# Kernel optimization log

Hardware: AMD Instinct MI355X
Metric: run time of the kernel (lower is better)

Reference implementation:

```python
import jax, jax.numpy as jnp
import numpy as np

K_HOPS = 10
ALPHA = 0.1


def setup_inputs() -> dict:
    key = jax.random.key(0)
    ks = jax.random.split(key, 12)
    B, H, N, IC, F, C = 4096, 5, 30, 256, 512, 4
    real = jax.random.normal(ks[0], (B, N, IC), jnp.float32)
    imag = jax.random.normal(ks[1], (B, N, IC), jnp.float32)
    graph = jax.random.normal(ks[2], (B, H, N, N), jnp.float32)
    def lin(k, fan_in, shape):
        s = 1.0 / np.sqrt(fan_in)
        return jax.random.uniform(k, shape, jnp.float32, -s, s)
    W1 = lin(ks[3], IC, (IC, F)); b1 = lin(ks[4], IC, (F,))
    W2 = lin(ks[5], F, (F, F));  b2 = lin(ks[6], F, (F,))
    Wl = lin(ks[7], F, (F, 1));  bl = lin(ks[8], F, (1,))
    Wc = lin(ks[9], N, (C, N));  bc = lin(ks[10], N, (C,))
    return {"real": real, "imag": imag, "graph": graph,
            "W1": W1, "b1": b1, "W2": W2, "b2": b2,
            "Wl": Wl, "bl": bl, "Wc": Wc, "bc": bc}


def _appnp(S, x):
    # x_{k+1} = alpha * x0 + (1 - alpha) * S @ x_k, K iterations
    x0 = x
    def step(h, _):
        h = ALPHA * x0 + (1.0 - ALPHA) * jnp.einsum('bij,bjf->bif', S, h)
        return h, None
    h, _ = jax.lax.scan(step, x, None, length=K_HOPS)
    return h


def _prop_matrix(graph):
    # adj = mean over frequency dim; edges = nonzero entries (weights discarded
    # by the original code), self loops added, symmetric gcn_norm with
    # degree = column sums; source->target flow => operator is transposed.
    adj = jnp.mean(graph, axis=1)                      # [B,N,N]
    M = (adj != 0).astype(graph.dtype)
    N = M.shape[-1]
    Mt = M + jnp.eye(N, dtype=graph.dtype)             # add self loops
    deg = jnp.sum(Mt, axis=-2)                         # in-degree (col sums) [B,N]
    dinv = jax.lax.rsqrt(deg)
    S = dinv[:, :, None] * jnp.swapaxes(Mt, -1, -2) * dinv[:, None, :]
    return S


def reference(real, imag, graph, W1, b1, W2, b2, Wl, bl, Wc, bc):
    S = _prop_matrix(graph)
    # layer 1: linear -> relu -> APPNP(K=10)
    x = jax.nn.relu(jnp.einsum('bni,if->bnf', real, W1) + b1)
    x = _appnp(S, x)
    # layer 2: linear -> relu -> APPNP(K=10)
    x = jax.nn.relu(jnp.einsum('bnf,fg->bng', x, W2) + b2)
    x = _appnp(S, x)
    # readout: per-node linear to scalar, relu, then Conv1d(30->C, k=1)
    x = jax.nn.relu(jnp.einsum('bnf,fo->bno', x, Wl)[..., 0] + bl[0])  # [B,N]
    out = jnp.einsum('bn,cn->bc', x, Wc) + bc                          # [B,C]
    return out
```

## Files before the change

### kernel.cpp

```cpp
#include <hip/hip_runtime.h>
#include <hip/hip_bf16.h>

typedef _Float16 f16;
typedef _Float16 f16x8 __attribute__((ext_vector_type(8)));
typedef _Float16 f16x4 __attribute__((ext_vector_type(4)));
typedef float f32x4 __attribute__((ext_vector_type(4)));

#define P_OFF   0
#define W1T_OFF 14745600
#define W2T_OFF 15007744

__global__ __launch_bounds__(256) void k_prep(const float* __restrict__ W1,
                                              const float* __restrict__ W2,
                                              f16* __restrict__ w1t,
                                              f16* __restrict__ w2t) {
    long id = (long)blockIdx.x * 256 + threadIdx.x;
    if (id < 131072) {
        int f = (int)(id >> 8), k = (int)(id & 255);
        w1t[id] = (f16)W1[k * 512 + f];
    } else {
        long i = id - 131072;
        int f = (int)(i >> 9), k = (int)(i & 511);
        w2t[i] = (f16)W2[k * 512 + f];
    }
}

__global__ __launch_bounds__(256) void k_prop(const float* __restrict__ graph,
                                              float* __restrict__ P) {
    __shared__ float MtS[4][990];
    __shared__ float dinvS[4][32];
    __shared__ f16 qhS[4][1024];
    __shared__ f16 qlS[4][1024];

    const int wv = threadIdx.x >> 6, lane = threadIdx.x & 63;
    const int lr = lane & 15, gq = lane >> 4;
    const long b = (long)blockIdx.x * 4 + wv;
    const float* g = graph + b * 4500;
    float* Mt = MtS[wv];
    float* dinv = dinvS[wv];
    f16* qh = qhS[wv];
    f16* ql = qlS[wv];

    for (int rep = 0; rep < 15; ++rep) {
        int e = rep * 64 + lane;
        if (e < 900) {
            float s = g[e] + g[900 + e] + g[1800 + e] + g[2700 + e] + g[3600 + e];
            int r = e / 30, c = e - r * 30;
            Mt[r * 33 + c] = ((s != 0.f) ? 1.f : 0.f) + ((r == c) ? 1.f : 0.f);
        }
    }
    __syncthreads();
    if (lane < 30) {
        float d = 0.f;
        #pragma unroll
        for (int r = 0; r < 30; ++r) d += Mt[r * 33 + lane];
        dinv[lane] = 1.0f / sqrtf(d);
    }
    __syncthreads();

    auto Sval = [&](int i, int j) -> float {
        if (i >= 30 || j >= 30) return 0.f;
        return dinv[i] * Mt[j * 33 + i] * dinv[j];
    };

    f16x8 sh[2], sl[2];
    #pragma unroll
    for (int mi = 0; mi < 2; ++mi)
        #pragma unroll
        for (int jj = 0; jj < 8; ++jj) {
            float v = Sval(mi * 16 + lr, gq * 8 + jj);
            f16 h = (f16)v;
            sh[mi][jj] = h;
            sl[mi][jj] = (f16)(v - (float)h);
        }

    f32x4 qd[2][2], racc[2][2];
    #pragma unroll
    for (int mi = 0; mi < 2; ++mi)
        #pragma unroll
        for (int ni = 0; ni < 2; ++ni)
            #pragma unroll
            for (int r = 0; r < 4; ++r) {
                int row = mi * 16 + gq * 4 + r, col = ni * 16 + lr;
                qd[mi][ni][r] = Sval(row, col);
                racc[mi][ni][r] = (row == col) ? 0.1f : 0.f;
            }

    float c = 0.1f;
    for (int k = 1; k <= 9; ++k) {
        c *= 0.9f;
        #pragma unroll
        for (int mi = 0; mi < 2; ++mi)
            #pragma unroll
            for (int ni = 0; ni < 2; ++ni) {
                racc[mi][ni] += c * qd[mi][ni];
                f16x4 hh, ll;
                #pragma unroll
                for (int r = 0; r < 4; ++r) {
                    float v = qd[mi][ni][r];
                    f16 h = (f16)v;
                    hh[r] = h;
                    ll[r] = (f16)(v - (float)h);
                }
                const int col = ni * 16 + lr, rowb = mi * 16 + gq * 4;
                *reinterpret_cast<f16x4*>(qh + col * 32 + rowb) = hh;
                *reinterpret_cast<f16x4*>(ql + col * 32 + rowb) = ll;
            }
        __syncthreads();
        f16x8 bh[2], bl[2];
        #pragma unroll
        for (int ni = 0; ni < 2; ++ni) {
            const int col = ni * 16 + lr;
            bh[ni] = *reinterpret_cast<const f16x8*>(qh + col * 32 + gq * 8);
            bl[ni] = *reinterpret_cast<const f16x8*>(ql + col * 32 + gq * 8);
        }
        #pragma unroll
        for (int mi = 0; mi < 2; ++mi)
            #pragma unroll
            for (int ni = 0; ni < 2; ++ni) {
                f32x4 d = {0.f, 0.f, 0.f, 0.f};
                d = __builtin_amdgcn_mfma_f32_16x16x32_f16(sh[mi], bh[ni], d, 0, 0, 0);
                d = __builtin_amdgcn_mfma_f32_16x16x32_f16(sh[mi], bl[ni], d, 0, 0, 0);
                d = __builtin_amdgcn_mfma_f32_16x16x32_f16(sl[mi], bh[ni], d, 0, 0, 0);
                qd[mi][ni] = d;
            }
        __syncthreads();
    }
    const float cf = 0.3486784401f;
    #pragma unroll
    for (int mi = 0; mi < 2; ++mi)
        #pragma unroll
        for (int ni = 0; ni < 2; ++ni)
            #pragma unroll
            for (int r = 0; r < 4; ++r) {
                int row = mi * 16 + gq * 4 + r, col = ni * 16 + lr;
                if (row < 30 && col < 30)
                    P[b * 900 + row * 30 + col] = racc[mi][ni][r] + cf * qd[mi][ni][r];
            }
}

#define SMEM_BYTES 150496
#define PF_OFF   131072
#define B1L_OFF  139264
#define B2L_OFF  141312
#define WLL_OFF  143360
#define RED_OFF  145408
#define VL_OFF   149504
#define ZL_OFF   150016

__global__ __launch_bounds__(512, 2) void k_main(
    const float* __restrict__ real, const f16* __restrict__ w1t,
    const f16* __restrict__ w2t, const float* __restrict__ b1,
    const float* __restrict__ b2, const float* __restrict__ wl,
    const float* __restrict__ bl, const float* __restrict__ wc,
    const float* __restrict__ bc, const float* __restrict__ Pws,
    float* __restrict__ out) {
    extern __shared__ char smem[];
    char*  buf = smem;
    f16*   Pf  = (f16*)(smem + PF_OFF);
    float* b1l = (float*)(smem + B1L_OFF);
    float* b2l = (float*)(smem + B2L_OFF);
    float* wll = (float*)(smem + WLL_OFF);
    float* red = (float*)(smem + RED_OFF);
    float* vl  = (float*)(smem + VL_OFF);
    float* zl  = (float*)(smem + ZL_OFF);

    const int tid  = threadIdx.x;
    const int lane = tid & 63;
    const int wv   = tid >> 6;
    const int gq   = lane >> 4;
    const int lr   = lane & 15;
    const int blk  = blockIdx.x;
    const long r0  = (long)blk * 120;

    #pragma unroll
    for (int s = 0; s < 8; ++s) {
        int id  = tid + s * 512;
        int row = id >> 5;
        int c8  = id & 31;
        int q = row >> 5, rr = row & 31;
        float4 v0 = {0.f,0.f,0.f,0.f}, v1 = {0.f,0.f,0.f,0.f};
        if (rr < 30) {
            const float* p = real + (r0 + q * 30 + rr) * 256 + c8 * 8;
            v0 = *reinterpret_cast<const float4*>(p);
            v1 = *reinterpret_cast<const float4*>(p + 4);
        }
        f16x8 h;
        h[0]=(f16)v0.x; h[1]=(f16)v0.y; h[2]=(f16)v0.z; h[3]=(f16)v0.w;
        h[4]=(f16)v1.x; h[5]=(f16)v1.y; h[6]=(f16)v1.z; h[7]=(f16)v1.w;
        *reinterpret_cast<f16x8*>(buf + row * 512 + ((c8 * 16) ^ ((row & 7) << 4))) = h;
    }
    #pragma unroll
    for (int s = 0; s < 8; ++s) {
        int e = tid + s * 512;
        int bb = e >> 10, idx = e & 1023, n = idx >> 5, kk = idx & 31;
        float p = (n < 30 && kk < 30) ? Pws[((long)blk * 4 + bb) * 900 + n * 30 + kk] : 0.f;
        Pf[e] = (f16)p;
    }
    b1l[tid] = b1[tid];
    b2l[tid] = b2[tid];
    wll[tid] = wl[tid];

    f32x4 acc[4][8];
    #pragma unroll
    for (int a = 0; a < 4; ++a)
        #pragma unroll
        for (int b = 0; b < 8; ++b) { f32x4 z = {0.f,0.f,0.f,0.f}; acc[a][b] = z; }
    __syncthreads();

    const f16* w1p = w1t + (wv * 64 + lr) * 256;
    f16x8 afA[4], afB[4];
    #pragma unroll
    for (int mi = 0; mi < 4; ++mi)
        afA[mi] = *reinterpret_cast<const f16x8*>(w1p + mi * 4096 + 0 * 32 + gq * 8);
    #pragma unroll
    for (int mi = 0; mi < 4; ++mi)
        afB[mi] = *reinterpret_cast<const f16x8*>(w1p + mi * 4096 + 1 * 32 + gq * 8);
    #pragma unroll
    for (int kc2 = 0; kc2 < 4; ++kc2) {
        {
            const int kc = 2 * kc2;
            f16x8 bf[8];
            #pragma unroll
            for (int ni = 0; ni < 8; ++ni) {
                const int row = ni * 16 + lr;
                bf[ni] = *reinterpret_cast<const f16x8*>(
                    buf + row * 512 + (((kc * 32 + gq * 8) * 2) ^ ((row & 7) << 4)));
            }
            #pragma unroll
            for (int mi = 0; mi < 4; ++mi)
                #pragma unroll
                for (int ni = 0; ni < 8; ++ni)
                    acc[mi][ni] = __builtin_amdgcn_mfma_f32_16x16x32_f16(afA[mi], bf[ni], acc[mi][ni], 0, 0, 0);
            if (kc + 2 < 8)
                #pragma unroll
                for (int mi = 0; mi < 4; ++mi)
                    afA[mi] = *reinterpret_cast<const f16x8*>(w1p + mi * 4096 + (kc + 2) * 32 + gq * 8);
        }
        {
            const int kc = 2 * kc2 + 1;
            f16x8 bf[8];
            #pragma unroll
            for (int ni = 0; ni < 8; ++ni) {
                const int row = ni * 16 + lr;
                bf[ni] = *reinterpret_cast<const f16x8*>(
                    buf + row * 512 + (((kc * 32 + gq * 8) * 2) ^ ((row & 7) << 4)));
            }
            #pragma unroll
            for (int mi = 0; mi < 4; ++mi)
                #pragma unroll
                for (int ni = 0; ni < 8; ++ni)
                    acc[mi][ni] = __builtin_amdgcn_mfma_f32_16x16x32_f16(afB[mi], bf[ni], acc[mi][ni], 0, 0, 0);
            if (kc + 2 < 8)
                #pragma unroll
                for (int mi = 0; mi < 4; ++mi)
                    afB[mi] = *reinterpret_cast<const f16x8*>(w1p + mi * 4096 + (kc + 2) * 32 + gq * 8);
        }
    }
    __syncthreads();

    #pragma unroll
    for (int mi = 0; mi < 4; ++mi) {
        const int featb = wv * 64 + mi * 16 + gq * 4;
        float b1v[4];
        #pragma unroll
        for (int j = 0; j < 4; ++j) b1v[j] = b1l[featb + j];
        #pragma unroll
        for (int ni = 0; ni < 8; ++ni) {
            const int node = ni * 16 + lr;
            f16x4 h;
            #pragma unroll
            for (int j = 0; j < 4; ++j)
                h[j] = (f16)fmaxf(acc[mi][ni][j] + b1v[j], 0.f);
            *reinterpret_cast<f16x4*>(
                buf + node * 1024 + ((featb * 2) ^ ((node & 7) << 4))) = h;
        }
    }
    #pragma unroll
    for (int a = 0; a < 4; ++a)
        #pragma unroll
        for (int b = 0; b < 8; ++b) { f32x4 z = {0.f,0.f,0.f,0.f}; acc[a][b] = z; }
    __syncthreads();

    const f16* w2p = w2t + (wv * 64 + lr) * 512;
    f16x8 bfA[4], bfB[4];
    #pragma unroll
    for (int ni = 0; ni < 4; ++ni)
        bfA[ni] = *reinterpret_cast<const f16x8*>(w2p + ni * 8192 + 0 * 32 + gq * 8);
    #pragma unroll
    for (int ni = 0; ni < 4; ++ni)
        bfB[ni] = *reinterpret_cast<const f16x8*>(w2p + ni * 8192 + 1 * 32 + gq * 8);
    #pragma unroll
    for (int kc2 = 0; kc2 < 8; ++kc2) {
        {
            const int kc = 2 * kc2;
            f16x8 af[8];
            #pragma unroll
            for (int mi = 0; mi < 8; ++mi) {
                const int row = mi * 16 + lr;
                af[mi] = *reinterpret_cast<const f16x8*>(
                    buf + row * 1024 + (((kc * 32 + gq * 8) * 2) ^ ((row & 7) << 4)));
            }
            #pragma unroll
            for (int mi = 0; mi < 8; ++mi)
                #pragma unroll
                for (int ni = 0; ni < 4; ++ni)
                    acc[ni][mi] = __builtin_amdgcn_mfma_f32_16x16x32_f16(af[mi], bfA[ni], acc[ni][mi], 0, 0, 0);
            if (kc + 2 < 16)
                #pragma unroll
                for (int ni = 0; ni < 4; ++ni)
                    bfA[ni] = *reinterpret_cast<const f16x8*>(w2p + ni * 8192 + (kc + 2) * 32 + gq * 8);
        }
        {
            const int kc = 2 * kc2 + 1;
            f16x8 af[8];
            #pragma unroll
            for (int mi = 0; mi < 8; ++mi) {
                const int row = mi * 16 + lr;
                af[mi] = *reinterpret_cast<const f16x8*>(
                    buf + row * 1024 + (((kc * 32 + gq * 8) * 2) ^ ((row & 7) << 4)));
            }
            #pragma unroll
            for (int mi = 0; mi < 8; ++mi)
                #pragma unroll
                for (int ni = 0; ni < 4; ++ni)
                    acc[ni][mi] = __builtin_amdgcn_mfma_f32_16x16x32_f16(af[mi], bfB[ni], acc[ni][mi], 0, 0, 0);
            if (kc + 2 < 16)
                #pragma unroll
                for (int ni = 0; ni < 4; ++ni)
                    bfB[ni] = *reinterpret_cast<const f16x8*>(w2p + ni * 8192 + (kc + 2) * 32 + gq * 8);
        }
    }
    __syncthreads();

    #pragma unroll
    for (int mi = 0; mi < 8; ++mi)
        #pragma unroll
        for (int ni = 0; ni < 4; ++ni) {
            const int feat  = wv * 64 + ni * 16 + lr;
            const int node0 = mi * 16 + gq * 4;
            f16x4 h;
            #pragma unroll
            for (int j = 0; j < 4; ++j) h[j] = (f16)acc[ni][mi][j];
            *reinterpret_cast<f16x4*>(
                buf + feat * 256 + ((node0 * 2) ^ ((feat & 7) << 4))) = h;
        }
    __syncthreads();

    {
        f16x8 pb[4][2];
        #pragma unroll
        for (int bb = 0; bb < 4; ++bb)
            #pragma unroll
            for (int ni = 0; ni < 2; ++ni)
                pb[bb][ni] = *reinterpret_cast<const f16x8*>(
                    Pf + bb * 1024 + (ni * 16 + lr) * 32 + gq * 8);
        float vacc[4][2];
        #pragma unroll
        for (int bb = 0; bb < 4; ++bb)
            #pragma unroll
            for (int ni = 0; ni < 2; ++ni) vacc[bb][ni] = 0.f;
        #pragma unroll
        for (int mi = 0; mi < 4; ++mi) {
            const int featb = wv * 64 + mi * 16;
            float b2v[4], wlv[4];
            #pragma unroll
            for (int j = 0; j < 4; ++j) {
                b2v[j] = b2l[featb + gq * 4 + j];
                wlv[j] = wll[featb + gq * 4 + j];
            }
            f16x8 au[4];
            #pragma unroll
            for (int bb = 0; bb < 4; ++bb) {
                const int feat = featb + lr;
                au[bb] = *reinterpret_cast<const f16x8*>(
                    buf + feat * 256 + ((bb * 64 + gq * 16) ^ ((feat & 7) << 4)));
            }
            #pragma unroll
            for (int bb = 0; bb < 4; ++bb)
                #pragma unroll
                for (int ni = 0; ni < 2; ++ni) {
                    f32x4 d = {0.f,0.f,0.f,0.f};
                    d = __builtin_amdgcn_mfma_f32_16x16x32_f16(au[bb], pb[bb][ni], d, 0, 0, 0);
                    #pragma unroll
                    for (int j = 0; j < 4; ++j) {
                        float y = fmaxf(d[j] + b2v[j], 0.f);
                        vacc[bb][ni] = fmaf(y, wlv[j], vacc[bb][ni]);
                    }
                }
        }
        #pragma unroll
        for (int bb = 0; bb < 4; ++bb)
            #pragma unroll
            for (int ni = 0; ni < 2; ++ni) {
                float v = vacc[bb][ni];
                v += __shfl_xor(v, 16);
                v += __shfl_xor(v, 32);
                if (lane < 16) red[wv * 128 + bb * 32 + ni * 16 + lr] = v;
            }
    }
    __syncthreads();
    if (tid < 128) {
        float s = 0.f;
        #pragma unroll
        for (int w = 0; w < 8; ++w) s += red[w * 128 + tid];
        vl[tid] = s;
    }
    __syncthreads();
    if (tid < 120) {
        const int bb = tid / 30, n = tid - bb * 30;
        const float* Pr = Pws + ((long)blk * 4 + bb) * 900 + n * 30;
        float z = bl[0];
        #pragma unroll
        for (int j = 0; j < 30; ++j) z = fmaf(Pr[j], vl[bb * 32 + j], z);
        zl[tid] = fmaxf(z, 0.f);
    }
    __syncthreads();
    if (tid < 16) {
        const int bb = tid >> 2, cc = tid & 3;
        float o = bc[cc];
        #pragma unroll
        for (int n = 0; n < 30; ++n) o = fmaf(zl[bb * 30 + n], wc[cc * 30 + n], o);
        out[((long)blk * 4 + bb) * 4 + cc] = o;
    }
}

extern "C" void kernel_launch(void* const* d_in, const int* in_sizes, int n_in,
                              void* d_out, int out_size, void* d_ws, size_t ws_size,
                              hipStream_t stream) {
    const float* real  = (const float*)d_in[0];
    const float* graph = (const float*)d_in[2];
    const float* W1    = (const float*)d_in[3];
    const float* b1    = (const float*)d_in[4];
    const float* W2    = (const float*)d_in[5];
    const float* b2    = (const float*)d_in[6];
    const float* Wl    = (const float*)d_in[7];
    const float* bl    = (const float*)d_in[8];
    const float* Wc    = (const float*)d_in[9];
    const float* bc    = (const float*)d_in[10];
    float* out = (float*)d_out;
    char*  ws  = (char*)d_ws;

    float* Pws = (float*)(ws + P_OFF);
    f16*   w1t = (f16*)(ws + W1T_OFF);
    f16*   w2t = (f16*)(ws + W2T_OFF);

    k_prep<<<1536, 256, 0, stream>>>(W1, W2, w1t, w2t);
    k_prop<<<1024, 256, 0, stream>>>(graph, Pws);
    (void)hipFuncSetAttribute((const void*)k_main,
                              hipFuncAttributeMaxDynamicSharedMemorySize, SMEM_BYTES);
    k_main<<<1024, 512, SMEM_BYTES, stream>>>(real, w1t, w2t, b1, b2, Wl, bl, Wc, bc,
                                              Pws, out);
}
```

Baseline: 185.8 us.

## Make k_main persistent over four tiles with pipelined streaming of input chunks

k_main now launches 256 blocks and each block loops over four 120-row tiles instead of one. The fp32 input is loaded in 64-column chunks into registers, converted and written into a double-buffered shared-memory slot while the MFMAs on the previous chunk run, and the next tile's first chunk is prefetched during the tail of the current tile. The swizzle is widened to 16 rows. This hides global load latency behind compute and amortises per-block setup, but with 256 blocks of two per CU the grid may not fill all CUs, and the extra barriers per chunk add sync cost.

```diff
diff --git a/kernel.cpp b/kernel.cpp
--- a/kernel.cpp
+++ b/kernel.cpp
@@ -139,7 +139,8 @@
             }
 }
 
-#define SMEM_BYTES 150496
+#define TILES 4
+#define SMEM_BYTES 150528
 #define PF_OFF   131072
 #define B1L_OFF  139264
 #define B2L_OFF  141312
@@ -171,257 +172,267 @@
     const int gq   = lane >> 4;
     const int lr   = lane & 15;
     const int blk  = blockIdx.x;
-    const long r0  = (long)blk * 120;
-
-    #pragma unroll
-    for (int s = 0; s < 8; ++s) {
-        int id  = tid + s * 512;
-        int row = id >> 5;
-        int c8  = id & 31;
-        int q = row >> 5, rr = row & 31;
-        float4 v0 = {0.f,0.f,0.f,0.f}, v1 = {0.f,0.f,0.f,0.f};
-        if (rr < 30) {
-            const float* p = real + (r0 + q * 30 + rr) * 256 + c8 * 8;
-            v0 = *reinterpret_cast<const float4*>(p);
-            v1 = *reinterpret_cast<const float4*>(p + 4);
-        }
-        f16x8 h;
-        h[0]=(f16)v0.x; h[1]=(f16)v0.y; h[2]=(f16)v0.z; h[3]=(f16)v0.w;
-        h[4]=(f16)v1.x; h[5]=(f16)v1.y; h[6]=(f16)v1.z; h[7]=(f16)v1.w;
-        *reinterpret_cast<f16x8*>(buf + row * 512 + ((c8 * 16) ^ ((row & 7) << 4))) = h;
-    }
-    #pragma unroll
-    for (int s = 0; s < 8; ++s) {
-        int e = tid + s * 512;
-        int bb = e >> 10, idx = e & 1023, n = idx >> 5, kk = idx & 31;
-        float p = (n < 30 && kk < 30) ? Pws[((long)blk * 4 + bb) * 900 + n * 30 + kk] : 0.f;
-        Pf[e] = (f16)p;
-    }
+
+    const int crow = tid >> 2;
+    const int cq   = tid & 3;
+    const bool cval = (crow & 31) < 30;
+    const long csrc = (long)(crow >> 5) * 30 + (crow & 31);
+
+    auto LOADC = [&](f32x4* r, int tt, int kc2) {
+        if (cval) {
+            const float* p = real + ((long)(blk * TILES + tt) * 120 + csrc) * 256
+                             + kc2 * 64 + cq * 16;
+            r[0] = *reinterpret_cast<const f32x4*>(p);
+            r[1] = *reinterpret_cast<const f32x4*>(p + 4);
+            r[2] = *reinterpret_cast<const f32x4*>(p + 8);
+            r[3] = *reinterpret_cast<const f32x4*>(p + 12);
+        }
+    };
+    auto WRITEC = [&](int slot, const f32x4* r) {
+        #pragma unroll
+        for (int h = 0; h < 2; ++h) {
+            f16x8 v;
+            #pragma unroll
+            for (int j = 0; j < 8; ++j)
+                v[j] = cval ? (f16)r[h * 2 + (j >> 2)][j & 3] : (f16)0.f;
+            *reinterpret_cast<f16x8*>(buf + slot * 16384 + crow * 128 +
+                ((cq * 32 + h * 16) ^ ((crow & 7) << 4))) = v;
+        }
+    };
+
     b1l[tid] = b1[tid];
     b2l[tid] = b2[tid];
     wll[tid] = wl[tid];
 
-    f32x4 acc[4][8];
-    #pragma unroll
-    for (int a = 0; a < 4; ++a)
-        #pragma unroll
-        for (int b = 0; b < 8; ++b) { f32x4 z = {0.f,0.f,0.f,0.f}; acc[a][b] = z; }
-    __syncthreads();
+    f32x4 cregA[4], cregB[4];
+    LOADC(cregA, 0, 0);
 
     const f16* w1p = w1t + (wv * 64 + lr) * 256;
-    f16x8 afA[4], afB[4];
-    #pragma unroll
-    for (int mi = 0; mi < 4; ++mi)
-        afA[mi] = *reinterpret_cast<const f16x8*>(w1p + mi * 4096 + 0 * 32 + gq * 8);
-    #pragma unroll
-    for (int mi = 0; mi < 4; ++mi)
-        afB[mi] = *reinterpret_cast<const f16x8*>(w1p + mi * 4096 + 1 * 32 + gq * 8);
-    #pragma unroll
-    for (int kc2 = 0; kc2 < 4; ++kc2) {
-        {
-            const int kc = 2 * kc2;
+    const f16* w2p = w2t + (wv * 64 + lr) * 512;
+
+    #pragma unroll 1
+    for (int t = 0; t < TILES; ++t) {
+        WRITEC(0, cregA);
+        LOADC(cregB, t, 1);
+        #pragma unroll
+        for (int s = 0; s < 8; ++s) {
+            int e = tid + s * 512;
+            int bb = e >> 10, idx = e & 1023, n = idx >> 5, kk = idx & 31;
+            float p = (n < 30 && kk < 31 && kk < 30)
+                ? Pws[((long)(blk * TILES + t) * 4 + bb) * 900 + n * 30 + kk] : 0.f;
+            Pf[e] = (f16)p;
+        }
+        __syncthreads();
+
+        f32x4 acc[4][8];
+        #pragma unroll
+        for (int a = 0; a < 4; ++a)
+            #pragma unroll
+            for (int b = 0; b < 8; ++b) { f32x4 z = {0.f,0.f,0.f,0.f}; acc[a][b] = z; }
+
+        #pragma unroll
+        for (int kc2 = 0; kc2 < 4; ++kc2) {
+            const int slot = kc2 & 1;
+            char* sb = buf + slot * 16384;
+            f16x8 wa[4], wb[4];
+            #pragma unroll
+            for (int mi = 0; mi < 4; ++mi) {
+                wa[mi] = *reinterpret_cast<const f16x8*>(w1p + mi * 4096 + kc2 * 64 + gq * 8);
+                wb[mi] = *reinterpret_cast<const f16x8*>(w1p + mi * 4096 + kc2 * 64 + 32 + gq * 8);
+            }
+            if (kc2 < 3) WRITEC(slot ^ 1, (kc2 & 1) ? cregA : cregB);
+            if (kc2 < 2) LOADC((kc2 & 1) ? cregB : cregA, t, kc2 + 2);
             f16x8 bf[8];
             #pragma unroll
             for (int ni = 0; ni < 8; ++ni) {
                 const int row = ni * 16 + lr;
                 bf[ni] = *reinterpret_cast<const f16x8*>(
-                    buf + row * 512 + (((kc * 32 + gq * 8) * 2) ^ ((row & 7) << 4)));
+                    sb + row * 128 + ((gq * 16) ^ ((row & 7) << 4)));
             }
             #pragma unroll
             for (int mi = 0; mi < 4; ++mi)
                 #pragma unroll
                 for (int ni = 0; ni < 8; ++ni)
-                    acc[mi][ni] = __builtin_amdgcn_mfma_f32_16x16x32_f16(afA[mi], bf[ni], acc[mi][ni], 0, 0, 0);
-            if (kc + 2 < 8)
-                #pragma unroll
-                for (int mi = 0; mi < 4; ++mi)
-                    afA[mi] = *reinterpret_cast<const f16x8*>(w1p + mi * 4096 + (kc + 2) * 32 + gq * 8);
-        }
-        {
-            const int kc = 2 * kc2 + 1;
-            f16x8 bf[8];
+                    acc[mi][ni] = __builtin_amdgcn_mfma_f32_16x16x32_f16(wa[mi], bf[ni], acc[mi][ni], 0, 0, 0);
             #pragma unroll
             for (int ni = 0; ni < 8; ++ni) {
                 const int row = ni * 16 + lr;
                 bf[ni] = *reinterpret_cast<const f16x8*>(
-                    buf + row * 512 + (((kc * 32 + gq * 8) * 2) ^ ((row & 7) << 4)));
+                    sb + row * 128 + ((64 + gq * 16) ^ ((row & 7) << 4)));
             }
             #pragma unroll
             for (int mi = 0; mi < 4; ++mi)
                 #pragma unroll
                 for (int ni = 0; ni < 8; ++ni)
-                    acc[mi][ni] = __builtin_amdgcn_mfma_f32_16x16x32_f16(afB[mi], bf[ni], acc[mi][ni], 0, 0, 0);
-            if (kc + 2 < 8)
-                #pragma unroll
-                for (int mi = 0; mi < 4; ++mi)
-                    afB[mi] = *reinterpret_cast<const f16x8*>(w1p + mi * 4096 + (kc + 2) * 32 + gq * 8);
-        }
-    }
-    __syncthreads();
-
-    #pragma unroll
-    for (int mi = 0; mi < 4; ++mi) {
-        const int featb = wv * 64 + mi * 16 + gq * 4;
-        float b1v[4];
-        #pragma unroll
-        for (int j = 0; j < 4; ++j) b1v[j] = b1l[featb + j];
-        #pragma unroll
-        for (int ni = 0; ni < 8; ++ni) {
-            const int node = ni * 16 + lr;
-            f16x4 h;
-            #pragma unroll
-            for (int j = 0; j < 4; ++j)
-                h[j] = (f16)fmaxf(acc[mi][ni][j] + b1v[j], 0.f);
-            *reinterpret_cast<f16x4*>(
-                buf + node * 1024 + ((featb * 2) ^ ((node & 7) << 4))) = h;
-        }
-    }
-    #pragma unroll
-    for (int a = 0; a < 4; ++a)
-        #pragma unroll
-        for (int b = 0; b < 8; ++b) { f32x4 z = {0.f,0.f,0.f,0.f}; acc[a][b] = z; }
-    __syncthreads();
-
-    const f16* w2p = w2t + (wv * 64 + lr) * 512;
-    f16x8 bfA[4], bfB[4];
-    #pragma unroll
-    for (int ni = 0; ni < 4; ++ni)
-        bfA[ni] = *reinterpret_cast<const f16x8*>(w2p + ni * 8192 + 0 * 32 + gq * 8);
-    #pragma unroll
-    for (int ni = 0; ni < 4; ++ni)
-        bfB[ni] = *reinterpret_cast<const f16x8*>(w2p + ni * 8192 + 1 * 32 + gq * 8);
-    #pragma unroll
-    for (int kc2 = 0; kc2 < 8; ++kc2) {
+                    acc[mi][ni] = __builtin_amdgcn_mfma_f32_16x16x32_f16(wb[mi], bf[ni], acc[mi][ni], 0, 0, 0);
+            __syncthreads();
+        }
+
+        #pragma unroll
+        for (int mi = 0; mi < 4; ++mi) {
+            const int featb = wv * 64 + mi * 16 + gq * 4;
+            float b1v[4];
+            #pragma unroll
+            for (int j = 0; j < 4; ++j) b1v[j] = b1l[featb + j];
+            #pragma unroll
+            for (int ni = 0; ni < 8; ++ni) {
+                const int node = ni * 16 + lr;
+                f16x4 h;
+                #pragma unroll
+                for (int j = 0; j < 4; ++j)
+                    h[j] = (f16)fmaxf(acc[mi][ni][j] + b1v[j], 0.f);
+                *reinterpret_cast<f16x4*>(
+                    buf + node * 1024 + ((featb * 2) ^ ((node & 15) << 4))) = h;
+            }
+        }
+        #pragma unroll
+        for (int a = 0; a < 4; ++a)
+            #pragma unroll
+            for (int b = 0; b < 8; ++b) { f32x4 z = {0.f,0.f,0.f,0.f}; acc[a][b] = z; }
+        __syncthreads();
+
+        f16x8 bfA[4], bfB[4];
+        #pragma unroll
+        for (int ni = 0; ni < 4; ++ni)
+            bfA[ni] = *reinterpret_cast<const f16x8*>(w2p + ni * 8192 + gq * 8);
+        #pragma unroll
+        for (int ni = 0; ni < 4; ++ni)
+            bfB[ni] = *reinterpret_cast<const f16x8*>(w2p + ni * 8192 + 32 + gq * 8);
+        #pragma unroll
+        for (int kc2 = 0; kc2 < 8; ++kc2) {
+            {
+                const int kc = 2 * kc2;
+                f16x8 af[8];
+                #pragma unroll
+                for (int mi = 0; mi < 8; ++mi) {
+                    const int row = mi * 16 + lr;
+                    af[mi] = *reinterpret_cast<const f16x8*>(
+                        buf + row * 1024 + (((kc * 32 + gq * 8) * 2) ^ ((row & 15) << 4)));
+                }
+                #pragma unroll
+                for (int mi = 0; mi < 8; ++mi)
+                    #pragma unroll
+                    for (int ni = 0; ni < 4; ++ni)
+                        acc[ni][mi] = __builtin_amdgcn_mfma_f32_16x16x32_f16(af[mi], bfA[ni], acc[ni][mi], 0, 0, 0);
+                if (kc + 2 < 16)
+                    #pragma unroll
+                    for (int ni = 0; ni < 4; ++ni)
+                        bfA[ni] = *reinterpret_cast<const f16x8*>(w2p + ni * 8192 + (kc + 2) * 32 + gq * 8);
+            }
+            {
+                const int kc = 2 * kc2 + 1;
+                f16x8 af[8];
+                #pragma unroll
+                for (int mi = 0; mi < 8; ++mi) {
+                    const int row = mi * 16 + lr;
+                    af[mi] = *reinterpret_cast<const f16x8*>(
+                        buf + row * 1024 + (((kc * 32 + gq * 8) * 2) ^ ((row & 15) << 4)));
+                }
+                #pragma unroll
+                for (int mi = 0; mi < 8; ++mi)
+                    #pragma unroll
+                    for (int ni = 0; ni < 4; ++ni)
+                        acc[ni][mi] = __builtin_amdgcn_mfma_f32_16x16x32_f16(af[mi], bfB[ni], acc[ni][mi], 0, 0, 0);
+                if (kc + 2 < 16)
+                    #pragma unroll
+                    for (int ni = 0; ni < 4; ++ni)
+                        bfB[ni] = *reinterpret_cast<const f16x8*>(w2p + ni * 8192 + (kc + 2) * 32 + gq * 8);
+            }
+        }
+        __syncthreads();
+
+        #pragma unroll
+        for (int mi = 0; mi < 8; ++mi)
+            #pragma unroll
+            for (int ni = 0; ni < 4; ++ni) {
+                const int feat  = wv * 64 + ni * 16 + lr;
+                const int node0 = mi * 16 + gq * 4;
+                f16x4 h;
+                #pragma unroll
+                for (int j = 0; j < 4; ++j) h[j] = (f16)acc[ni][mi][j];
+                *reinterpret_cast<f16x4*>(
+                    buf + feat * 256 + ((node0 * 2) ^ ((feat & 15) << 4))) = h;
+            }
+        if (t + 1 < TILES) LOADC(cregA, t + 1, 0);
+        __syncthreads();
+
         {
-            const int kc = 2 * kc2;
-            f16x8 af[8];
-            #pragma unroll
-            for (int mi = 0; mi < 8; ++mi) {
-                const int row = mi * 16 + lr;
-                af[mi] = *reinterpret_cast<const f16x8*>(
-                    buf + row * 1024 + (((kc * 32 + gq * 8) * 2) ^ ((row & 7) << 4)));
-            }
-            #pragma unroll
-            for (int mi = 0; mi < 8; ++mi)
-                #pragma unroll
-                for (int ni = 0; ni < 4; ++ni)
-                    acc[ni][mi] = __builtin_amdgcn_mfma_f32_16x16x32_f16(af[mi], bfA[ni], acc[ni][mi], 0, 0, 0);
-            if (kc + 2 < 16)
-                #pragma unroll
-                for (int ni = 0; ni < 4; ++ni)
-                    bfA[ni] = *reinterpret_cast<const f16x8*>(w2p + ni * 8192 + (kc + 2) * 32 + gq * 8);
-        }
-        {
-            const int kc = 2 * kc2 + 1;
-            f16x8 af[8];
-            #pragma unroll
-            for (int mi = 0; mi < 8; ++mi) {
-                const int row = mi * 16 + lr;
-                af[mi] = *reinterpret_cast<const f16x8*>(
-                    buf + row * 1024 + (((kc * 32 + gq * 8) * 2) ^ ((row & 7) << 4)));
-            }
-            #pragma unroll
-            for (int mi = 0; mi < 8; ++mi)
-                #pragma unroll
-                for (int ni = 0; ni < 4; ++ni)
-                    acc[ni][mi] = __builtin_amdgcn_mfma_f32_16x16x32_f16(af[mi], bfB[ni], acc[ni][mi], 0, 0, 0);
-            if (kc + 2 < 16)
-                #pragma unroll
-                for (int ni = 0; ni < 4; ++ni)
-                    bfB[ni] = *reinterpret_cast<const f16x8*>(w2p + ni * 8192 + (kc + 2) * 32 + gq * 8);
-        }
-    }
-    __syncthreads();
-
-    #pragma unroll
-    for (int mi = 0; mi < 8; ++mi)
-        #pragma unroll
-        for (int ni = 0; ni < 4; ++ni) {
-            const int feat  = wv * 64 + ni * 16 + lr;
-            const int node0 = mi * 16 + gq * 4;
-            f16x4 h;
-            #pragma unroll
-            for (int j = 0; j < 4; ++j) h[j] = (f16)acc[ni][mi][j];
-            *reinterpret_cast<f16x4*>(
-                buf + feat * 256 + ((node0 * 2) ^ ((feat & 7) << 4))) = h;
-        }
-    __syncthreads();
-
-    {
-        f16x8 pb[4][2];
-        #pragma unroll
-        for (int bb = 0; bb < 4; ++bb)
-            #pragma unroll
-            for (int ni = 0; ni < 2; ++ni)
-                pb[bb][ni] = *reinterpret_cast<const f16x8*>(
-                    Pf + bb * 1024 + (ni * 16 + lr) * 32 + gq * 8);
-        float vacc[4][2];
-        #pragma unroll
-        for (int bb = 0; bb < 4; ++bb)
-            #pragma unroll
-            for (int ni = 0; ni < 2; ++ni) vacc[bb][ni] = 0.f;
-        #pragma unroll
-        for (int mi = 0; mi < 4; ++mi) {
-            const int featb = wv * 64 + mi * 16;
-            float b2v[4], wlv[4];
-            #pragma unroll
-            for (int j = 0; j < 4; ++j) {
-                b2v[j] = b2l[featb + gq * 4 + j];
-                wlv[j] = wll[featb + gq * 4 + j];
-            }
-            f16x8 au[4];
-            #pragma unroll
-            for (int bb = 0; bb < 4; ++bb) {
-                const int feat = featb + lr;
-                au[bb] = *reinterpret_cast<const f16x8*>(
-                    buf + feat * 256 + ((bb * 64 + gq * 16) ^ ((feat & 7) << 4)));
-            }
+            f16x8 pb[4][2];
             #pragma unroll
             for (int bb = 0; bb < 4; ++bb)
                 #pragma unroll
+                for (int ni = 0; ni < 2; ++ni)
+                    pb[bb][ni] = *reinterpret_cast<const f16x8*>(
+                        Pf + bb * 1024 + (ni * 16 + lr) * 32 + gq * 8);
+            float vacc[4][2];
+            #pragma unroll
+            for (int bb = 0; bb < 4; ++bb)
+                #pragma unroll
+                for (int ni = 0; ni < 2; ++ni) vacc[bb][ni] = 0.f;
+            #pragma unroll
+            for (int mi = 0; mi < 4; ++mi) {
+                const int featb = wv * 64 + mi * 16;
+                float b2v[4], wlv[4];
+                #pragma unroll
+                for (int j = 0; j < 4; ++j) {
+                    b2v[j] = b2l[featb + gq * 4 + j];
+                    wlv[j] = wll[featb + gq * 4 + j];
+                }
+                f16x8 au[4];
+                #pragma unroll
+                for (int bb = 0; bb < 4; ++bb) {
+                    const int feat = featb + lr;
+                    au[bb] = *reinterpret_cast<const f16x8*>(
+                        buf + feat * 256 + ((bb * 64 + gq * 16) ^ ((feat & 15) << 4)));
+                }
+                #pragma unroll
+                for (int bb = 0; bb < 4; ++bb)
+                    #pragma unroll
+                    for (int ni = 0; ni < 2; ++ni) {
+                        f32x4 d = {0.f,0.f,0.f,0.f};
+                        d = __builtin_amdgcn_mfma_f32_16x16x32_f16(au[bb], pb[bb][ni], d, 0, 0, 0);
+                        #pragma unroll
+                        for (int j = 0; j < 4; ++j) {
+                            float y = fmaxf(d[j] + b2v[j], 0.f);
+                            vacc[bb][ni] = fmaf(y, wlv[j], vacc[bb][ni]);
+                        }
+                    }
+            }
+            #pragma unroll
+            for (int bb = 0; bb < 4; ++bb)
+                #pragma unroll
                 for (int ni = 0; ni < 2; ++ni) {
-                    f32x4 d = {0.f,0.f,0.f,0.f};
-                    d = __builtin_amdgcn_mfma_f32_16x16x32_f16(au[bb], pb[bb][ni], d, 0, 0, 0);
-                    #pragma unroll
-                    for (int j = 0; j < 4; ++j) {
-                        float y = fmaxf(d[j] + b2v[j], 0.f);
-                        vacc[bb][ni] = fmaf(y, wlv[j], vacc[bb][ni]);
-                    }
-                }
-        }
-        #pragma unroll
-        for (int bb = 0; bb < 4; ++bb)
-            #pragma unroll
-            for (int ni = 0; ni < 2; ++ni) {
-                float v = vacc[bb][ni];
-                v += __shfl_xor(v, 16);
-                v += __shfl_xor(v, 32);
-                if (lane < 16) red[wv * 128 + bb * 32 + ni * 16 + lr] = v;
-            }
-    }
-    __syncthreads();
-    if (tid < 128) {
-        float s = 0.f;
-        #pragma unroll
-        for (int w = 0; w < 8; ++w) s += red[w * 128 + tid];
-        vl[tid] = s;
-    }
-    __syncthreads();
-    if (tid < 120) {
-        const int bb = tid / 30, n = tid - bb * 30;
-        const float* Pr = Pws + ((long)blk * 4 + bb) * 900 + n * 30;
-        float z = bl[0];
-        #pragma unroll
-        for (int j = 0; j < 30; ++j) z = fmaf(Pr[j], vl[bb * 32 + j], z);
-        zl[tid] = fmaxf(z, 0.f);
-    }
-    __syncthreads();
-    if (tid < 16) {
-        const int bb = tid >> 2, cc = tid & 3;
-        float o = bc[cc];
-        #pragma unroll
-        for (int n = 0; n < 30; ++n) o = fmaf(zl[bb * 30 + n], wc[cc * 30 + n], o);
-        out[((long)blk * 4 + bb) * 4 + cc] = o;
+                    float v = vacc[bb][ni];
+                    v += __shfl_xor(v, 16);
+                    v += __shfl_xor(v, 32);
+                    if (lane < 16) red[wv * 128 + bb * 32 + ni * 16 + lr] = v;
+                }
+        }
+        __syncthreads();
+        if (tid < 128) {
+            float s = 0.f;
+            #pragma unroll
+            for (int w = 0; w < 8; ++w) s += red[w * 128 + tid];
+            vl[tid] = s;
+        }
+        __syncthreads();
+        if (tid < 120) {
+            const int bb = tid / 30, n = tid - bb * 30;
+            const float* Pr = Pws + ((long)(blk * TILES + t) * 4 + bb) * 900 + n * 30;
+            float z = bl[0];
+            #pragma unroll
+            for (int j = 0; j < 30; ++j) z = fmaf(Pr[j], vl[bb * 32 + j], z);
+            zl[tid] = fmaxf(z, 0.f);
+        }
+        __syncthreads();
+        if (tid < 16) {
+            const int bb = tid >> 2, cc = tid & 3;
+            float o = bc[cc];
+            #pragma unroll
+            for (int n = 0; n < 30; ++n) o = fmaf(zl[bb * 30 + n], wc[cc * 30 + n], o);
+            out[((long)(blk * TILES + t) * 4 + bb) * 4 + cc] = o;
+        }
+        __syncthreads();
     }
 }
 
@@ -449,6 +460,6 @@
     k_prop<<<1024, 256, 0, stream>>>(graph, Pws);
     (void)hipFuncSetAttribute((const void*)k_main,
                               hipFuncAttributeMaxDynamicSharedMemorySize, SMEM_BYTES);
-    k_main<<<1024, 512, SMEM_BYTES, stream>>>(real, w1t, w2t, b1, b2, Wl, bl, Wc, bc,
-                                              Pws, out);
+    k_main<<<256, 512, SMEM_BYTES, stream>>>(real, w1t, w2t, b1, b2, Wl, bl, Wc, bc,
+                                             Pws, out);
 }
```

Result: slower. 484.2 us (+160.6%).

## Stage input rows via direct global-to-LDS loads and widen LDS swizzle

Applied to the files above, without the earlier changes.

The fp32 input tile is now copied straight from global memory into LDS with global_load_lds, using an XOR-swizzled lane mapping, instead of being loaded into registers, converted to fp16 and stored. The layer-1 GEMM converts fp32 to fp16 when it reads LDS, and it loads W1 fragments per k-chunk rather than double-buffering them. The swizzle widens from 8 to 16 rows, the P matrix gets padded rows (stride 40) to reduce bank conflicts, and s_setprio wraps the MFMA bursts. The aim is to cut register pressure and VALU conversion work on the load path. The cost is twice the LDS traffic per B fragment and a larger shared-memory footprint.

```diff
diff --git a/kernel.cpp b/kernel.cpp
--- a/kernel.cpp
+++ b/kernel.cpp
@@ -139,14 +139,14 @@
             }
 }
 
-#define SMEM_BYTES 150496
+#define SMEM_BYTES 152576
 #define PF_OFF   131072
-#define B1L_OFF  139264
-#define B2L_OFF  141312
-#define WLL_OFF  143360
-#define RED_OFF  145408
-#define VL_OFF   149504
-#define ZL_OFF   150016
+#define B1L_OFF  141312
+#define B2L_OFF  143360
+#define WLL_OFF  145408
+#define RED_OFF  147456
+#define VL_OFF   151552
+#define ZL_OFF   152064
 
 __global__ __launch_bounds__(512, 2) void k_main(
     const float* __restrict__ real, const f16* __restrict__ w1t,
@@ -173,29 +173,33 @@
     const int blk  = blockIdx.x;
     const long r0  = (long)blk * 120;
 
-    #pragma unroll
-    for (int s = 0; s < 8; ++s) {
-        int id  = tid + s * 512;
-        int row = id >> 5;
-        int c8  = id & 31;
-        int q = row >> 5, rr = row & 31;
-        float4 v0 = {0.f,0.f,0.f,0.f}, v1 = {0.f,0.f,0.f,0.f};
+    const float* rbase = real + r0 * 256;
+    #pragma unroll
+    for (int i = 0; i < 16; ++i) {
+        const int row = wv + 8 * i;
+        const int rr  = row & 31;
         if (rr < 30) {
-            const float* p = real + (r0 + q * 30 + rr) * 256 + c8 * 8;
-            v0 = *reinterpret_cast<const float4*>(p);
-            v1 = *reinterpret_cast<const float4*>(p + 4);
-        }
-        f16x8 h;
-        h[0]=(f16)v0.x; h[1]=(f16)v0.y; h[2]=(f16)v0.z; h[3]=(f16)v0.w;
-        h[4]=(f16)v1.x; h[5]=(f16)v1.y; h[6]=(f16)v1.z; h[7]=(f16)v1.w;
-        *reinterpret_cast<f16x8*>(buf + row * 512 + ((c8 * 16) ^ ((row & 7) << 4))) = h;
+            const float* gp = rbase + ((long)((row >> 5) * 30 + rr)) * 256
+                              + ((lane ^ wv) << 2);
+            __builtin_amdgcn_global_load_lds(
+                (const __attribute__((address_space(1))) unsigned int*)gp,
+                (__attribute__((address_space(3))) unsigned int*)(buf + row * 1024),
+                16, 0, 0);
+        }
+    }
+    {
+        const int i   = tid >> 6;
+        const int row = ((i >> 1) << 5) + 30 + (i & 1);
+        f32x4 z = {0.f, 0.f, 0.f, 0.f};
+        *reinterpret_cast<f32x4*>(buf + row * 1024 + (tid & 63) * 16) = z;
     }
     #pragma unroll
     for (int s = 0; s < 8; ++s) {
         int e = tid + s * 512;
         int bb = e >> 10, idx = e & 1023, n = idx >> 5, kk = idx & 31;
-        float p = (n < 30 && kk < 30) ? Pws[((long)blk * 4 + bb) * 900 + n * 30 + kk] : 0.f;
-        Pf[e] = (f16)p;
+        float p = (n < 30 && kk < 30)
+            ? Pws[((long)blk * 4 + bb) * 900 + n * 30 + kk] : 0.f;
+        Pf[bb * 1280 + n * 40 + kk] = (f16)p;
     }
     b1l[tid] = b1[tid];
     b2l[tid] = b2[tid];
@@ -209,53 +213,33 @@
     __syncthreads();
 
     const f16* w1p = w1t + (wv * 64 + lr) * 256;
-    f16x8 afA[4], afB[4];
-    #pragma unroll
-    for (int mi = 0; mi < 4; ++mi)
-        afA[mi] = *reinterpret_cast<const f16x8*>(w1p + mi * 4096 + 0 * 32 + gq * 8);
-    #pragma unroll
-    for (int mi = 0; mi < 4; ++mi)
-        afB[mi] = *reinterpret_cast<const f16x8*>(w1p + mi * 4096 + 1 * 32 + gq * 8);
-    #pragma unroll
-    for (int kc2 = 0; kc2 < 4; ++kc2) {
-        {
-            const int kc = 2 * kc2;
-            f16x8 bf[8];
-            #pragma unroll
-            for (int ni = 0; ni < 8; ++ni) {
-                const int row = ni * 16 + lr;
-                bf[ni] = *reinterpret_cast<const f16x8*>(
-                    buf + row * 512 + (((kc * 32 + gq * 8) * 2) ^ ((row & 7) << 4)));
-            }
-            #pragma unroll
-            for (int mi = 0; mi < 4; ++mi)
-                #pragma unroll
-                for (int ni = 0; ni < 8; ++ni)
-                    acc[mi][ni] = __builtin_amdgcn_mfma_f32_16x16x32_f16(afA[mi], bf[ni], acc[mi][ni], 0, 0, 0);
-            if (kc + 2 < 8)
-                #pragma unroll
-                for (int mi = 0; mi < 4; ++mi)
-                    afA[mi] = *reinterpret_cast<const f16x8*>(w1p + mi * 4096 + (kc + 2) * 32 + gq * 8);
-        }
-        {
-            const int kc = 2 * kc2 + 1;
-            f16x8 bf[8];
-            #pragma unroll
-            for (int ni = 0; ni < 8; ++ni) {
-                const int row = ni * 16 + lr;
-                bf[ni] = *reinterpret_cast<const f16x8*>(
-                    buf + row * 512 + (((kc * 32 + gq * 8) * 2) ^ ((row & 7) << 4)));
-            }
-            #pragma unroll
-            for (int mi = 0; mi < 4; ++mi)
-                #pragma unroll
-                for (int ni = 0; ni < 8; ++ni)
-                    acc[mi][ni] = __builtin_amdgcn_mfma_f32_16x16x32_f16(afB[mi], bf[ni], acc[mi][ni], 0, 0, 0);
-            if (kc + 2 < 8)
-                #pragma unroll
-                for (int mi = 0; mi < 4; ++mi)
-                    afB[mi] = *reinterpret_cast<const f16x8*>(w1p + mi * 4096 + (kc + 2) * 32 + gq * 8);
-        }
+    #pragma unroll
+    for (int kc = 0; kc < 8; ++kc) {
+        f16x8 wa[4];
+        #pragma unroll
+        for (int mi = 0; mi < 4; ++mi)
+            wa[mi] = *reinterpret_cast<const f16x8*>(w1p + mi * 4096 + kc * 32 + gq * 8);
+        f16x8 bf[8];
+        #pragma unroll
+        for (int ni = 0; ni < 8; ++ni) {
+            const int row = ni * 16 + lr;
+            const int cb  = kc * 128 + gq * 32;
+            f32x4 a0 = *reinterpret_cast<const f32x4*>(
+                buf + row * 1024 + (cb ^ ((row & 7) << 4)));
+            f32x4 a1 = *reinterpret_cast<const f32x4*>(
+                buf + row * 1024 + ((cb + 16) ^ ((row & 7) << 4)));
+            f16x8 h;
+            h[0]=(f16)a0[0]; h[1]=(f16)a0[1]; h[2]=(f16)a0[2]; h[3]=(f16)a0[3];
+            h[4]=(f16)a1[0]; h[5]=(f16)a1[1]; h[6]=(f16)a1[2]; h[7]=(f16)a1[3];
+            bf[ni] = h;
+        }
+        __builtin_amdgcn_s_setprio(1);
+        #pragma unroll
+        for (int mi = 0; mi < 4; ++mi)
+            #pragma unroll
+            for (int ni = 0; ni < 8; ++ni)
+                acc[mi][ni] = __builtin_amdgcn_mfma_f32_16x16x32_f16(wa[mi], bf[ni], acc[mi][ni], 0, 0, 0);
+        __builtin_amdgcn_s_setprio(0);
     }
     __syncthreads();
 
@@ -273,7 +257,7 @@
             for (int j = 0; j < 4; ++j)
                 h[j] = (f16)fmaxf(acc[mi][ni][j] + b1v[j], 0.f);
             *reinterpret_cast<f16x4*>(
-                buf + node * 1024 + ((featb * 2) ^ ((node & 7) << 4))) = h;
+                buf + node * 1024 + ((featb * 2) ^ ((node & 15) << 4))) = h;
         }
     }
     #pragma unroll
@@ -286,10 +270,10 @@
     f16x8 bfA[4], bfB[4];
     #pragma unroll
     for (int ni = 0; ni < 4; ++ni)
-        bfA[ni] = *reinterpret_cast<const f16x8*>(w2p + ni * 8192 + 0 * 32 + gq * 8);
+        bfA[ni] = *reinterpret_cast<const f16x8*>(w2p + ni * 8192 + gq * 8);
     #pragma unroll
     for (int ni = 0; ni < 4; ++ni)
-        bfB[ni] = *reinterpret_cast<const f16x8*>(w2p + ni * 8192 + 1 * 32 + gq * 8);
+        bfB[ni] = *reinterpret_cast<const f16x8*>(w2p + ni * 8192 + 32 + gq * 8);
     #pragma unroll
     for (int kc2 = 0; kc2 < 8; ++kc2) {
         {
@@ -299,13 +283,15 @@
             for (int mi = 0; mi < 8; ++mi) {
                 const int row = mi * 16 + lr;
                 af[mi] = *reinterpret_cast<const f16x8*>(
-                    buf + row * 1024 + (((kc * 32 + gq * 8) * 2) ^ ((row & 7) << 4)));
-            }
+                    buf + row * 1024 + (((kc * 32 + gq * 8) * 2) ^ ((row & 15) << 4)));
+            }
+            __builtin_amdgcn_s_setprio(1);
             #pragma unroll
             for (int mi = 0; mi < 8; ++mi)
                 #pragma unroll
                 for (int ni = 0; ni < 4; ++ni)
                     acc[ni][mi] = __builtin_amdgcn_mfma_f32_16x16x32_f16(af[mi], bfA[ni], acc[ni][mi], 0, 0, 0);
+            __builtin_amdgcn_s_setprio(0);
             if (kc + 2 < 16)
                 #pragma unroll
                 for (int ni = 0; ni < 4; ++ni)
@@ -318,13 +304,15 @@
             for (int mi = 0; mi < 8; ++mi) {
                 const int row = mi * 16 + lr;
                 af[mi] = *reinterpret_cast<const f16x8*>(
-                    buf + row * 1024 + (((kc * 32 + gq * 8) * 2) ^ ((row & 7) << 4)));
-            }
+                    buf + row * 1024 + (((kc * 32 + gq * 8) * 2) ^ ((row & 15) << 4)));
+            }
+            __builtin_amdgcn_s_setprio(1);
             #pragma unroll
             for (int mi = 0; mi < 8; ++mi)
                 #pragma unroll
                 for (int ni = 0; ni < 4; ++ni)
                     acc[ni][mi] = __builtin_amdgcn_mfma_f32_16x16x32_f16(af[mi], bfB[ni], acc[ni][mi], 0, 0, 0);
+            __builtin_amdgcn_s_setprio(0);
             if (kc + 2 < 16)
                 #pragma unroll
                 for (int ni = 0; ni < 4; ++ni)
@@ -343,7 +331,7 @@
             #pragma unroll
             for (int j = 0; j < 4; ++j) h[j] = (f16)acc[ni][mi][j];
             *reinterpret_cast<f16x4*>(
-                buf + feat * 256 + ((node0 * 2) ^ ((feat & 7) << 4))) = h;
+                buf + feat * 256 + ((node0 * 2) ^ ((feat & 15) << 4))) = h;
         }
     __syncthreads();
 
@@ -354,7 +342,7 @@
             #pragma unroll
             for (int ni = 0; ni < 2; ++ni)
                 pb[bb][ni] = *reinterpret_cast<const f16x8*>(
-                    Pf + bb * 1024 + (ni * 16 + lr) * 32 + gq * 8);
+                    Pf + bb * 1280 + (ni * 16 + lr) * 40 + gq * 8);
         float vacc[4][2];
         #pragma unroll
         for (int bb = 0; bb < 4; ++bb)
@@ -374,7 +362,7 @@
             for (int bb = 0; bb < 4; ++bb) {
                 const int feat = featb + lr;
                 au[bb] = *reinterpret_cast<const f16x8*>(
-                    buf + feat * 256 + ((bb * 64 + gq * 16) ^ ((feat & 7) << 4)));
+                    buf + feat * 256 + ((bb * 64 + gq * 16) ^ ((feat & 15) << 4)));
             }
             #pragma unroll
             for (int bb = 0; bb < 4; ++bb)
```

Measured after the change: 184.3 us. No clear change (-0.8%).
